# Performance work log

Hardware: AMD Instinct MI355X
Metric: run time of the kernel (lower is better)

Reference implementation:

```python
import jax, jax.numpy as jnp
import numpy as np

NUM_POINTS = 16384
OVERSAMPLE = 3
IMPORTANCE_RATIO = 0.75


def point_sample(feat, coords):
    """grid_sample(bilinear, align_corners=False, zero padding) at [0,1]^2 coords.
    feat: (N, C, H, W); coords: (N, P, 2) with coords[...,0]=x (width), [...,1]=y.
    Returns (N, C, P)."""
    N, C, H, W = feat.shape
    # grid_sample with g = 2c-1, align_corners=False -> pixel = c*size - 0.5
    x = coords[..., 0] * W - 0.5
    y = coords[..., 1] * H - 0.5
    x0 = jnp.floor(x)
    y0 = jnp.floor(y)
    x1 = x0 + 1.0
    y1 = y0 + 1.0
    wx1 = x - x0
    wx0 = 1.0 - wx1
    wy1 = y - y0
    wy0 = 1.0 - wy1
    featf = feat.reshape(N, C, H * W)

    def gather(yi, xi):
        valid = (xi >= 0) & (xi <= W - 1) & (yi >= 0) & (yi <= H - 1)
        xic = jnp.clip(xi, 0, W - 1).astype(jnp.int32)
        yic = jnp.clip(yi, 0, H - 1).astype(jnp.int32)
        idx = yic * W + xic  # (N, P)
        v = jnp.take_along_axis(featf, idx[:, None, :], axis=2)  # (N, C, P)
        return v * valid[:, None, :].astype(feat.dtype)

    out = (gather(y0, x0) * (wy0 * wx0)[:, None, :]
           + gather(y0, x1) * (wy0 * wx1)[:, None, :]
           + gather(y1, x0) * (wy1 * wx0)[:, None, :]
           + gather(y1, x1) * (wy1 * wx1)[:, None, :])
    return out


def calculate_uncertainty(logits):
    """logits: (N, C, P) -> (N, P) uncertainty = top2 - top1 (<= 0)."""
    if logits.shape[1] == 1:
        return -jnp.abs(logits)[:, 0, :]
    top2 = jax.lax.top_k(jnp.moveaxis(logits, 1, -1), 2)[0]  # (N, P, 2)
    return top2[..., 1] - top2[..., 0]


def sample_point_coords(coarse_logits):
    """get_uncertain_point_coords_with_randomness (torch.no_grad branch)."""
    N = coarse_logits.shape[0]
    num_sampled = NUM_POINTS * OVERSAMPLE
    num_imp = int(IMPORTANCE_RATIO * NUM_POINTS)
    num_rand = NUM_POINTS - num_imp
    k1, k2 = jax.random.split(jax.random.key(7))
    cand = jax.random.uniform(k1, (N, num_sampled, 2), dtype=jnp.float32)
    cand_logits = point_sample(coarse_logits, cand)  # (N, C, S)
    unc = calculate_uncertainty(cand_logits)  # (N, S)
    idx = jax.lax.top_k(unc, num_imp)[1]  # (N, num_imp)
    imp = jnp.take_along_axis(cand, idx[..., None], axis=1)  # (N, num_imp, 2)
    rand = jax.random.uniform(k2, (N, num_rand, 2), dtype=jnp.float32)
    return jnp.concatenate([imp, rand], axis=1)  # (N, P, 2)


def point_head(fine, coarse_pts, w0, b0, w1, b1, w2, b2, wp, bp):
    x = jnp.concatenate([fine, coarse_pts], axis=1)  # (N, nin+C, P)
    for w, b in ((w0, b0), (w1, b1), (w2, b2)):
        x = jax.nn.relu(jnp.einsum('oc,ncp->nop', w, x) + b[None, :, None])
        x = jnp.concatenate([x, coarse_pts], axis=1)  # coarse_pred_each_layer
    return jnp.einsum('oc,ncp->nop', wp, x) + bp[None, :, None]  # (N, C, P)


def setup_inputs() -> dict:
    key = jax.random.key(0)
    ks = jax.random.split(key, 8)
    N, C, Hc, Wc = 8, 19, 64, 64
    nin, Hf, Wf = 256, 128, 128
    fin = nin + C  # 275
    return {
        'coarse_sem_seg_logits': jax.random.normal(ks[0], (N, C, Hc, Wc), jnp.float32),
        'features': jax.random.normal(ks[1], (N, nin, Hf, Wf), jnp.float32),
        'w0': jax.random.normal(ks[2], (nin, fin), jnp.float32) * (2.0 / fin) ** 0.5,
        'b0': jnp.zeros((nin,), jnp.float32),
        'w1': jax.random.normal(ks[3], (nin, fin), jnp.float32) * (2.0 / fin) ** 0.5,
        'b1': jnp.zeros((nin,), jnp.float32),
        'w2': jax.random.normal(ks[4], (nin, fin), jnp.float32) * (2.0 / fin) ** 0.5,
        'b2': jnp.zeros((nin,), jnp.float32),
        'wp': jax.random.normal(ks[5], (C, fin), jnp.float32) * 0.001,
        'bp': jnp.zeros((C,), jnp.float32),
    }


def reference(coarse_sem_seg_logits, features, w0, b0, w1, b1, w2, b2, wp, bp):
    # training-mode forward of PointRendSemSegHead
    point_coords = jax.lax.stop_gradient(
        sample_point_coords(jax.lax.stop_gradient(coarse_sem_seg_logits)))
    coarse_pts = point_sample(coarse_sem_seg_logits, point_coords)  # (N, C, P)
    fine_pts = point_sample(features, point_coords)  # (N, nin, P)
    point_logits = point_head(fine_pts, coarse_pts, w0, b0, w1, b1, w2, b2, wp, bp)
    return coarse_sem_seg_logits, point_logits, point_coords
```

## Files before the change

kernel.cpp:

```cpp
#include <hip/hip_runtime.h>
#include <stdint.h>

#pragma clang fp contract(off)

#define NB    8
#define CCH   19
#define CSTR  20
#define FCH   256
#define FIN   275
#define KP    288
#define NPTS  16384
#define NSAMP 49152
#define NIMP  12288
#define NRAND 4096
#define SORT_M 65536
#define CHUNK  8192
#define TP    64
#define XROW  640
#define WBF_OFF (4u << 20)
#define CTR_OFF (4718592u)
#define FTR_OFF (8u << 20)
#define FTR_BYTES (134217728ull / 2)

typedef __attribute__((ext_vector_type(8))) short bf16x8;
typedef __attribute__((ext_vector_type(4))) float f32x4;

__host__ __device__ __forceinline__ uint32_t rotl32(uint32_t v, int r) {
  return (v << r) | (v >> (32 - r));
}

__host__ __device__ __forceinline__ void tf2x32(uint32_t k0, uint32_t k1,
                                                uint32_t x0, uint32_t x1,
                                                uint32_t* o0, uint32_t* o1) {
  const uint32_t ks2 = k0 ^ k1 ^ 0x1BD11BDAu;
  x0 += k0; x1 += k1;
#define TF_R(r) { x0 += x1; x1 = rotl32(x1, (r)); x1 ^= x0; }
  TF_R(13) TF_R(15) TF_R(26) TF_R(6)
  x0 += k1;  x1 += ks2 + 1u;
  TF_R(17) TF_R(29) TF_R(16) TF_R(24)
  x0 += ks2; x1 += k0 + 2u;
  TF_R(13) TF_R(15) TF_R(26) TF_R(6)
  x0 += k0;  x1 += k1 + 3u;
  TF_R(17) TF_R(29) TF_R(16) TF_R(24)
  x0 += k1;  x1 += ks2 + 4u;
  TF_R(13) TF_R(15) TF_R(26) TF_R(6)
  x0 += ks2; x1 += k0 + 5u;
#undef TF_R
  *o0 = x0; *o1 = x1;
}

__device__ __forceinline__ float u01_at(uint32_t k0, uint32_t k1, uint32_t i) {
  uint32_t o0, o1;
  tf2x32(k0, k1, 0u, i, &o0, &o1);
  const uint32_t b = o0 ^ o1;
  const float f = __uint_as_float((b >> 9) | 0x3f800000u) - 1.0f;
  return fmaxf(0.0f, f);
}

__device__ __forceinline__ unsigned short f2bf(float f) {
  const uint32_t u = __float_as_uint(f);
  return (unsigned short)((u + 0x7fffu + ((u >> 16) & 1u)) >> 16);
}

__device__ __forceinline__ float bf2f(unsigned short h) {
  return __uint_as_float((uint32_t)h << 16);
}

template <int SZ>
__device__ __forceinline__ void interp(float cx, float cy, int* off, float* wgt) {
  const float X = cx * (float)SZ - 0.5f, Y = cy * (float)SZ - 0.5f;
  const float x0f = floorf(X), y0f = floorf(Y);
  const float fx = X - x0f, fy = Y - y0f;
  const float wx0 = 1.0f - fx, wy0 = 1.0f - fy;
  const int x0 = (int)x0f, y0 = (int)y0f;
  const int x0c = min(max(x0, 0), SZ - 1), x1c = min(max(x0 + 1, 0), SZ - 1);
  const int y0c = min(max(y0, 0), SZ - 1), y1c = min(max(y0 + 1, 0), SZ - 1);
  const bool vx0 = (x0 >= 0) & (x0 <= SZ - 1), vx1 = (x0 >= -1) & (x0 <= SZ - 2);
  const bool vy0 = (y0 >= 0) & (y0 <= SZ - 1), vy1 = (y0 >= -1) & (y0 <= SZ - 2);
  off[0] = y0c * SZ + x0c; wgt[0] = (vy0 & vx0) ? wy0 * wx0 : 0.0f;
  off[1] = y0c * SZ + x1c; wgt[1] = (vy0 & vx1) ? wy0 * fx  : 0.0f;
  off[2] = y1c * SZ + x0c; wgt[2] = (vy1 & vx0) ? fy  * wx0 : 0.0f;
  off[3] = y1c * SZ + x1c; wgt[3] = (vy1 & vx1) ? fy  * fx  : 0.0f;
}

__global__ __launch_bounds__(256) void ctr_transpose(
    const float* __restrict__ coarse, float* __restrict__ ctr) {
  __shared__ float tile[CCH][257];
  const int b = blockIdx.x;
  const int nn = b >> 4, px0 = (b & 15) * 256;
  const int t = threadIdx.x;
  const float* src = coarse + (size_t)nn * (CCH * 4096) + px0;
#pragma unroll
  for (int c = 0; c < CCH; ++c) tile[c][t] = src[c * 4096 + t];
  __syncthreads();
  float v[CSTR];
#pragma unroll
  for (int c = 0; c < CCH; ++c) v[c] = tile[c][t];
  v[19] = 0.0f;
  float* dst = ctr + ((size_t)(nn << 12) + px0 + t) * CSTR;
#pragma unroll
  for (int k = 0; k < 5; ++k) {
    f32x4 x; x[0] = v[4*k]; x[1] = v[4*k+1]; x[2] = v[4*k+2]; x[3] = v[4*k+3];
    *(f32x4*)(dst + 4 * k) = x;
  }
}

__global__ __launch_bounds__(256) void fusedA(
    const float* __restrict__ feats, unsigned short* __restrict__ ftr,
    const float* __restrict__ ctr, unsigned long long* __restrict__ keys,
    const float* __restrict__ w0, const float* __restrict__ w1,
    const float* __restrict__ w2, const float* __restrict__ wpw,
    unsigned short* __restrict__ wbf, unsigned short* __restrict__ wpb,
    uint32_t k1a, uint32_t k1b, int use_tr) {
  __shared__ unsigned short tile[64][66];
  const int bid = blockIdx.x;
  const int t = threadIdx.x;

  if (bid < 8192) {
    if (!use_tr) return;
    const int nn = bid >> 10;
    const int ct = (bid >> 8) & 3;
    const int pt = bid & 255;
    const int c0 = ct * 64, p0 = pt * 64;
    const float* src = feats + ((size_t)nn << 22);
#pragma unroll 4
    for (int k = 0; k < 16; ++k) {
      const int c = 4 * k + (t >> 6);
      const int p = t & 63;
      tile[p][c] = f2bf(src[((size_t)(c0 + c) << 14) + p0 + p]);
    }
    __syncthreads();
    const int p = t >> 2, q = t & 3;
    const int cb = q * 16;
    uint32_t w[8];
#pragma unroll
    for (int m = 0; m < 8; ++m)
      w[m] = (uint32_t)tile[p][cb + 2 * m] | ((uint32_t)tile[p][cb + 2 * m + 1] << 16);
    unsigned short* dst = ftr + ((((size_t)nn << 14) + p0 + p) << 8) + c0 + cb;
    *(uint4*)(dst)     = make_uint4(w[0], w[1], w[2], w[3]);
    *(uint4*)(dst + 8) = make_uint4(w[4], w[5], w[6], w[7]);
  } else if (bid < 10240) {
    const int tid = (bid - 8192) * 256 + t;
    const int nn = tid >> 16, s = tid & (SORT_M - 1);
    if (s >= NSAMP) { keys[tid] = 0xFFFFFFFFFFFFFFFFull; return; }
    const uint32_t ci = (uint32_t)(((unsigned)nn * NSAMP + (unsigned)s) * 2);
    const float cx = u01_at(k1a, k1b, ci);
    const float cy = u01_at(k1a, k1b, ci + 1);
    const float X = cx * 64.0f - 0.5f, Y = cy * 64.0f - 0.5f;
    const float x0f = floorf(X), y0f = floorf(Y);
    const float fx = X - x0f, fy = Y - y0f;
    const float wx0 = 1.0f - fx, wy0 = 1.0f - fy;
    const int x0 = (int)x0f, y0 = (int)y0f;
    const int x0c = min(max(x0, 0), 63), x1c = min(max(x0 + 1, 0), 63);
    const int y0c = min(max(y0, 0), 63), y1c = min(max(y0 + 1, 0), 63);
    const bool vx0 = (x0 >= 0) & (x0 <= 63), vx1 = (x0 >= -1) & (x0 <= 62);
    const bool vy0 = (y0 >= 0) & (y0 <= 63), vy1 = (y0 >= -1) & (y0 <= 62);
    const float w00 = (vy0 & vx0) ? wy0 * wx0 : 0.0f;
    const float w01 = (vy0 & vx1) ? wy0 * fx  : 0.0f;
    const float w10 = (vy1 & vx0) ? fy  * wx0 : 0.0f;
    const float w11 = (vy1 & vx1) ? fy  * fx  : 0.0f;
    const float* rb = ctr + ((size_t)nn << 12) * CSTR;
    const float* r0 = rb + (size_t)(y0c * 64 + x0c) * CSTR;
    const float* r1 = rb + (size_t)(y0c * 64 + x1c) * CSTR;
    const float* r2 = rb + (size_t)(y1c * 64 + x0c) * CSTR;
    const float* r3 = rb + (size_t)(y1c * 64 + x1c) * CSTR;
    float m1 = -3.402823466e38f, m2 = -3.402823466e38f;
#pragma unroll
    for (int k = 0; k < 5; ++k) {
      const f32x4 x0v = *(const f32x4*)(r0 + 4 * k);
      const f32x4 x1v = *(const f32x4*)(r1 + 4 * k);
      const f32x4 x2v = *(const f32x4*)(r2 + 4 * k);
      const f32x4 x3v = *(const f32x4*)(r3 + 4 * k);
#pragma unroll
      for (int e = 0; e < 4; ++e) {
        const int c = 4 * k + e;
        if (c < CCH) {
          const float v = ((x0v[e] * w00 + x1v[e] * w01) + x2v[e] * w10) + x3v[e] * w11;
          if (v > m1) { m2 = m1; m1 = v; } else if (v > m2) { m2 = v; }
        }
      }
    }
    const float unc = m2 - m1;
    const uint32_t b = __float_as_uint(unc);
    const uint32_t asc = (b & 0x80000000u) ? ~b : (b | 0x80000000u);
    keys[tid] = ((unsigned long long)(~asc) << 32) | (uint32_t)s;
  } else {
    const int i = (bid - 10240) * 256 + t;
    if (i < 3 * 256 * KP) {
      const int L = i / (256 * KP);
      const int rem = i - L * (256 * KP);
      const int o = rem / KP, k = rem - o * KP;
      const float* W = (L == 0) ? w0 : (L == 1) ? w1 : w2;
      wbf[i] = (k < FIN) ? f2bf(W[o * FIN + k]) : (unsigned short)0;
    } else {
      const int j = i - 3 * 256 * KP;
      const int o = j / KP, k = j - o * KP;
      wpb[j] = (o < CCH && k < FIN) ? f2bf(wpw[o * FIN + k]) : (unsigned short)0;
    }
  }
}

__global__ __launch_bounds__(1024) void bitonic_local(unsigned long long* __restrict__ keys) {
  __shared__ unsigned long long s[CHUNK];
  const int cb = blockIdx.x;
  unsigned long long* a = keys + (size_t)cb * CHUNK;
  const unsigned gbase = (unsigned)(cb * CHUNK) & (SORT_M - 1);
  for (int i = threadIdx.x; i < CHUNK; i += 1024) s[i] = a[i];
  __syncthreads();
  for (int k = 2; k <= CHUNK; k <<= 1) {
    for (int j = k >> 1; j > 0; j >>= 1) {
      for (int pid = threadIdx.x; pid < CHUNK / 2; pid += 1024) {
        const int i = ((pid & ~(j - 1)) << 1) | (pid & (j - 1));
        const int l = i | j;
        const bool up = (((gbase + i) & k) == 0);
        const unsigned long long x = s[i], y = s[l];
        if ((x > y) == up) { s[i] = y; s[l] = x; }
      }
      __syncthreads();
    }
  }
  for (int i = threadIdx.x; i < CHUNK; i += 1024) a[i] = s[i];
}

__global__ __launch_bounds__(256) void bitonic_global(unsigned long long* __restrict__ keys,
                                                      int k, int j, int ppb_shift) {
  const int t = blockIdx.x * blockDim.x + threadIdx.x;
  const int b = t >> ppb_shift, pid = t & ((1 << ppb_shift) - 1);
  const int i = ((pid & ~(j - 1)) << 1) | (pid & (j - 1));
  const int l = i | j;
  const bool up = ((i & k) == 0);
  unsigned long long* a = keys + ((size_t)b << 16);
  const unsigned long long x = a[i], y = a[l];
  if ((x > y) == up) { a[i] = y; a[l] = x; }
}

__global__ __launch_bounds__(1024) void bitonic_finish(unsigned long long* __restrict__ keys,
                                                       int k) {
  __shared__ unsigned long long s[CHUNK];
  const int cb = blockIdx.x;
  unsigned long long* a = keys + (size_t)cb * CHUNK;
  const unsigned gi0 = (unsigned)(cb * CHUNK) & (SORT_M - 1);
  for (int i = threadIdx.x; i < CHUNK; i += 1024) s[i] = a[i];
  __syncthreads();
  const bool up = ((gi0 & k) == 0);
  for (int j = CHUNK >> 1; j > 0; j >>= 1) {
    for (int pid = threadIdx.x; pid < CHUNK / 2; pid += 1024) {
      const int i = ((pid & ~(j - 1)) << 1) | (pid & (j - 1));
      const int l = i | j;
      const unsigned long long x = s[i], y = s[l];
      if ((x > y) == up) { s[i] = y; s[l] = x; }
    }
    __syncthreads();
  }
  for (int i = threadIdx.x; i < CHUNK; i += 1024) a[i] = s[i];
}

__global__ __launch_bounds__(1024) void finlow_coords(
    const unsigned long long* __restrict__ keys, float* __restrict__ outc,
    uint32_t k1a, uint32_t k1b, uint32_t k2a, uint32_t k2b) {
  __shared__ unsigned long long s[CHUNK];
  const int nn = blockIdx.x >> 1, half = blockIdx.x & 1;
  const unsigned long long* a = keys + ((size_t)nn << 16) + half * CHUNK;
  for (int i = threadIdx.x; i < CHUNK; i += 1024) s[i] = a[i];
  __syncthreads();
  for (int j = CHUNK >> 1; j > 0; j >>= 1) {
    for (int pid = threadIdx.x; pid < CHUNK / 2; pid += 1024) {
      const int i = ((pid & ~(j - 1)) << 1) | (pid & (j - 1));
      const int l = i | j;
      const unsigned long long x = s[i], y = s[l];
      if (x > y) { s[i] = y; s[l] = x; }
    }
    __syncthreads();
  }
  const int pb = half * CHUNK;
  for (int q = threadIdx.x; q < CHUNK; q += 1024) {
    const int p = pb + q;
    float cx, cy;
    if (p < NIMP) {
      const unsigned idx = (unsigned)(s[q] & 0xFFFFFFFFu);
      const uint32_t ci = ((unsigned)nn * NSAMP + idx) * 2;
      cx = u01_at(k1a, k1b, ci);
      cy = u01_at(k1a, k1b, ci + 1);
    } else {
      const uint32_t ri = ((unsigned)nn * NRAND + (unsigned)(p - NIMP)) * 2;
      cx = u01_at(k2a, k2b, ri);
      cy = u01_at(k2a, k2b, ri + 1);
    }
    float* o = outc + (((size_t)nn << 14) + p) * 2;
    o[0] = cx; o[1] = cy;
  }
}

template <int USE_TR>
__global__ __launch_bounds__(512, 4) void fused_mfma(
    const float* __restrict__ coarse, const float* __restrict__ feats,
    const unsigned short* __restrict__ ftr, const float* __restrict__ ctr,
    const float* __restrict__ b0, const float* __restrict__ b1,
    const float* __restrict__ b2, const float* __restrict__ bp,
    const unsigned short* __restrict__ wbf, const unsigned short* __restrict__ wpb,
    const float* __restrict__ pc, float* __restrict__ outl) {
  __shared__ __align__(16) unsigned short xp[TP * (XROW / 2)];

  const int t = threadIdx.x;
  const int bid = ((int)blockIdx.x & 7) * 256 + ((int)blockIdx.x >> 3);
  const int nn = bid >> 8;
  const int pbase = (bid & 255) * TP;

  int offF[4]; float wgtF[4];
  int offC[4]; float wgtC[4];
  int offFc[4]; float wgtFc[4];
  {
    const float2 c = *(const float2*)(pc + ((size_t)nn * NPTS + pbase + (t >> 3)) * 2);
    interp<128>(c.x, c.y, offF, wgtF);
  }
  {
    const float2 c = *(const float2*)(pc + ((size_t)nn * NPTS + pbase + (t & 63)) * 2);
    interp<64>(c.x, c.y, offC, wgtC);
    if (!USE_TR) interp<128>(c.x, c.y, offFc, wgtFc);
  }

  if (USE_TR) {
    const int p = t >> 3, q = t & 7;
    const unsigned short* base = ftr + ((size_t)nn << 22) + q * 32;
    const unsigned short* n0 = base + ((size_t)offF[0] << 8);
    const unsigned short* n1 = base + ((size_t)offF[1] << 8);
    const unsigned short* n2 = base + ((size_t)offF[2] << 8);
    const unsigned short* n3 = base + ((size_t)offF[3] << 8);
    const float g0 = wgtF[0], g1 = wgtF[1], g2 = wgtF[2], g3 = wgtF[3];
    const unsigned swzp = (unsigned)(p & 7) << 4;
#pragma unroll
    for (int m = 0; m < 4; ++m) {
      const bf16x8 a = *(const bf16x8*)(n0 + m * 8);
      const bf16x8 bq = *(const bf16x8*)(n1 + m * 8);
      const bf16x8 c = *(const bf16x8*)(n2 + m * 8);
      const bf16x8 d = *(const bf16x8*)(n3 + m * 8);
      uint32_t u[4];
#pragma unroll
      for (int e = 0; e < 4; ++e) {
        float v0 = fmaf(bf2f((unsigned short)a[2 * e]), g0,
                   fmaf(bf2f((unsigned short)bq[2 * e]), g1,
                   fmaf(bf2f((unsigned short)c[2 * e]), g2,
                        bf2f((unsigned short)d[2 * e]) * g3)));
        float v1 = fmaf(bf2f((unsigned short)a[2 * e + 1]), g0,
                   fmaf(bf2f((unsigned short)bq[2 * e + 1]), g1,
                   fmaf(bf2f((unsigned short)c[2 * e + 1]), g2,
                        bf2f((unsigned short)d[2 * e + 1]) * g3)));
        u[e] = (uint32_t)f2bf(v0) | ((uint32_t)f2bf(v1) << 16);
      }
      *(uint4*)((char*)xp + p * XROW + (((unsigned)((q * 32 + m * 8) * 2)) ^ swzp)) =
          make_uint4(u[0], u[1], u[2], u[3]);
    }
    if (t < TP) {
      const int pp = t;
      const float* rb = ctr + ((size_t)nn << 12) * CSTR;
      const float* r0 = rb + (size_t)offC[0] * CSTR;
      const float* r1 = rb + (size_t)offC[1] * CSTR;
      const float* r2 = rb + (size_t)offC[2] * CSTR;
      const float* r3 = rb + (size_t)offC[3] * CSTR;
      const float h0 = wgtC[0], h1 = wgtC[1], h2 = wgtC[2], h3 = wgtC[3];
      unsigned short hs[32];
#pragma unroll
      for (int k = 0; k < 5; ++k) {
        const f32x4 x0v = *(const f32x4*)(r0 + 4 * k);
        const f32x4 x1v = *(const f32x4*)(r1 + 4 * k);
        const f32x4 x2v = *(const f32x4*)(r2 + 4 * k);
        const f32x4 x3v = *(const f32x4*)(r3 + 4 * k);
#pragma unroll
        for (int e = 0; e < 4; ++e) {
          const int c = 4 * k + e;
          if (c < CCH)
            hs[c] = f2bf(fmaf(x0v[e], h0, fmaf(x1v[e], h1,
                         fmaf(x2v[e], h2, x3v[e] * h3))));
        }
      }
#pragma unroll
      for (int c = CCH; c < 32; ++c) hs[c] = 0;
      const unsigned swzc = (unsigned)(pp & 7) << 4;
#pragma unroll
      for (int k = 0; k < 4; ++k) {
        uint4 u;
        u.x = (uint32_t)hs[8*k]   | ((uint32_t)hs[8*k+1] << 16);
        u.y = (uint32_t)hs[8*k+2] | ((uint32_t)hs[8*k+3] << 16);
        u.z = (uint32_t)hs[8*k+4] | ((uint32_t)hs[8*k+5] << 16);
        u.w = (uint32_t)hs[8*k+6] | ((uint32_t)hs[8*k+7] << 16);
        *(uint4*)((char*)xp + pp * XROW + (((unsigned)(512 + 16 * k)) ^ swzc)) = u;
      }
    }
  } else {
    for (int i = t; i < (KP / 2) * TP; i += 512) {
      const int p = i & (TP - 1);
      const int c0 = (i >> 6) * 2;
      float v0 = 0.0f, v1 = 0.0f;
      if (c0 < FCH) {
        const float* fb0 = feats + ((size_t)nn << 22) + ((size_t)c0 << 14);
        const float* fb1 = fb0 + 16384;
        v0 = ((fb0[offFc[0]] * wgtFc[0] + fb0[offFc[1]] * wgtFc[1])
             + fb0[offFc[2]] * wgtFc[2]) + fb0[offFc[3]] * wgtFc[3];
        v1 = ((fb1[offFc[0]] * wgtFc[0] + fb1[offFc[1]] * wgtFc[1])
             + fb1[offFc[2]] * wgtFc[2]) + fb1[offFc[3]] * wgtFc[3];
      } else if (c0 < FIN) {
        const float* cb0 = coarse + (size_t)nn * (CCH * 4096) + (size_t)(c0 - FCH) * 4096;
        v0 = ((cb0[offC[0]] * wgtC[0] + cb0[offC[1]] * wgtC[1])
             + cb0[offC[2]] * wgtC[2]) + cb0[offC[3]] * wgtC[3];
        if (c0 + 1 < FIN) {
          const float* cb1 = cb0 + 4096;
          v1 = ((cb1[offC[0]] * wgtC[0] + cb1[offC[1]] * wgtC[1])
               + cb1[offC[2]] * wgtC[2]) + cb1[offC[3]] * wgtC[3];
        }
      }
      const uint32_t u = (uint32_t)f2bf(v0) | ((uint32_t)f2bf(v1) << 16);
      *(uint32_t*)((char*)xp + p * XROW + (((unsigned)(c0 * 2)) ^ ((unsigned)(p & 7) << 4))) = u;
    }
  }

  const int lane = t & 63, wave = t >> 6;
  const int wm = wave & 3, wn = wave >> 2;
  const int l15 = lane & 15, g = lane >> 4;
  const unsigned swz = (unsigned)(l15 & 7) << 4;
  const char* xpB = (const char*)xp;

#pragma unroll
  for (int L = 0; L < 3; ++L) {
    __syncthreads();
    const float* Bv = (L == 0) ? b0 : (L == 1) ? b1 : b2;
    const unsigned short* wL = wbf + (size_t)L * (256 * KP);
    const unsigned short* wbase = wL + (size_t)(wm * 64 + l15) * KP + g * 8;

    f32x4 acc[4][2];
#pragma unroll
    for (int mt = 0; mt < 4; ++mt)
#pragma unroll
      for (int nt = 0; nt < 2; ++nt) acc[mt][nt] = (f32x4)(0.0f);

    bf16x8 a0 = *(const bf16x8*)(wbase + 0 * 16 * KP);
    bf16x8 a1 = *(const bf16x8*)(wbase + 1 * 16 * KP);
    bf16x8 a2 = *(const bf16x8*)(wbase + 2 * 16 * KP);
    bf16x8 a3 = *(const bf16x8*)(wbase + 3 * 16 * KP);
    for (int ks = 0; ks < 9; ++ks) {
      const bf16x8 c0v = a0, c1v = a1, c2v = a2, c3v = a3;
      if (ks < 8) {
        a0 = *(const bf16x8*)(wbase + 0 * 16 * KP + (ks + 1) * 32);
        a1 = *(const bf16x8*)(wbase + 1 * 16 * KP + (ks + 1) * 32);
        a2 = *(const bf16x8*)(wbase + 2 * 16 * KP + (ks + 1) * 32);
        a3 = *(const bf16x8*)(wbase + 3 * 16 * KP + (ks + 1) * 32);
      }
      const unsigned kb = (unsigned)(ks * 64 + g * 16) ^ swz;
      const bf16x8 q0 = *(const bf16x8*)(xpB + (wn * 32 + 0 + l15) * XROW + kb);
      const bf16x8 q1 = *(const bf16x8*)(xpB + (wn * 32 + 16 + l15) * XROW + kb);
      acc[0][0] = __builtin_amdgcn_mfma_f32_16x16x32_bf16(c0v, q0, acc[0][0], 0, 0, 0);
      acc[1][0] = __builtin_amdgcn_mfma_f32_16x16x32_bf16(c1v, q0, acc[1][0], 0, 0, 0);
      acc[2][0] = __builtin_amdgcn_mfma_f32_16x16x32_bf16(c2v, q0, acc[2][0], 0, 0, 0);
      acc[3][0] = __builtin_amdgcn_mfma_f32_16x16x32_bf16(c3v, q0, acc[3][0], 0, 0, 0);
      acc[0][1] = __builtin_amdgcn_mfma_f32_16x16x32_bf16(c0v, q1, acc[0][1], 0, 0, 0);
      acc[1][1] = __builtin_amdgcn_mfma_f32_16x16x32_bf16(c1v, q1, acc[1][1], 0, 0, 0);
      acc[2][1] = __builtin_amdgcn_mfma_f32_16x16x32_bf16(c2v, q1, acc[2][1], 0, 0, 0);
      acc[3][1] = __builtin_amdgcn_mfma_f32_16x16x32_bf16(c3v, q1, acc[3][1], 0, 0, 0);
    }
    __syncthreads();

#pragma unroll
    for (int mt = 0; mt < 4; ++mt) {
      const int ch0 = wm * 64 + mt * 16 + (g << 2);
      const float4 bv = *(const float4*)(Bv + ch0);
#pragma unroll
      for (int nt = 0; nt < 2; ++nt) {
        const int p = wn * 32 + nt * 16 + l15;
        const f32x4 v = acc[mt][nt];
        const unsigned short h0 = f2bf(fmaxf(v[0] + bv.x, 0.0f));
        const unsigned short h1 = f2bf(fmaxf(v[1] + bv.y, 0.0f));
        const unsigned short h2 = f2bf(fmaxf(v[2] + bv.z, 0.0f));
        const unsigned short h3 = f2bf(fmaxf(v[3] + bv.w, 0.0f));
        uint2 u;
        u.x = (uint32_t)h0 | ((uint32_t)h1 << 16);
        u.y = (uint32_t)h2 | ((uint32_t)h3 << 16);
        *(uint2*)((char*)xp + p * XROW + (((unsigned)(ch0 * 2)) ^ swz)) = u;
      }
    }
  }
  __syncthreads();

  const int hmt = wave >> 2, hnt = wave & 3;
  const unsigned short* hbase = wpb + (size_t)(hmt * 16 + l15) * KP + g * 8;
  f32x4 hacc = (f32x4)(0.0f);
  for (int ks = 0; ks < 9; ++ks) {
    const unsigned kb = (unsigned)(ks * 64 + g * 16) ^ swz;
    const bf16x8 ha = *(const bf16x8*)(hbase + ks * 32);
    const bf16x8 hb = *(const bf16x8*)(xpB + (hnt * 16 + l15) * XROW + kb);
    hacc = __builtin_amdgcn_mfma_f32_16x16x32_bf16(ha, hb, hacc, 0, 0, 0);
  }
  const int p = pbase + hnt * 16 + l15;
#pragma unroll
  for (int j = 0; j < 4; ++j) {
    const int ch = hmt * 16 + (g << 2) + j;
    if (ch < CCH)
      outl[((size_t)nn * CCH + ch) * NPTS + p] = hacc[j] + bp[ch];
  }
}

extern "C" void kernel_launch(void* const* d_in, const int* in_sizes, int n_in,
                              void* d_out, int out_size, void* d_ws, size_t ws_size,
                              hipStream_t stream) {
  const float* coarse = (const float*)d_in[0];
  const float* feats  = (const float*)d_in[1];
  const float* w0 = (const float*)d_in[2]; const float* b0 = (const float*)d_in[3];
  const float* w1 = (const float*)d_in[4]; const float* b1 = (const float*)d_in[5];
  const float* w2 = (const float*)d_in[6]; const float* b2 = (const float*)d_in[7];
  const float* wp = (const float*)d_in[8]; const float* bp = (const float*)d_in[9];

  float* out0 = (float*)d_out;
  float* outL = out0 + 622592;
  float* outC = outL + 2490368;

  unsigned long long* keys = (unsigned long long*)d_ws;
  unsigned short* wbf = (unsigned short*)((char*)d_ws + WBF_OFF);
  unsigned short* wpb = wbf + 3 * 256 * KP;
  float* ctr = (float*)((char*)d_ws + CTR_OFF);
  unsigned short* ftr = (unsigned short*)((char*)d_ws + FTR_OFF);
  const int use_tr = (ws_size >= (size_t)FTR_OFF + FTR_BYTES) ? 1 : 0;

  uint32_t k1a, k1b, k2a, k2b;
  tf2x32(0u, 7u, 0u, 0u, &k1a, &k1b);
  tf2x32(0u, 7u, 0u, 1u, &k2a, &k2b);

  hipMemcpyAsync(out0, coarse, 622592 * sizeof(float),
                 hipMemcpyDeviceToDevice, stream);

  ctr_transpose<<<128, 256, 0, stream>>>(coarse, ctr);

  fusedA<<<11140, 256, 0, stream>>>(feats, ftr, ctr, keys,
                                    w0, w1, w2, wp, wbf, wpb, k1a, k1b, use_tr);

  bitonic_local<<<64, 1024, 0, stream>>>(keys);
  bitonic_global<<<1024, 256, 0, stream>>>(keys, 16384, 8192, 15);
  bitonic_finish<<<64, 1024, 0, stream>>>(keys, 16384);
  bitonic_global<<<1024, 256, 0, stream>>>(keys, 32768, 16384, 15);
  bitonic_global<<<1024, 256, 0, stream>>>(keys, 32768, 8192, 15);
  bitonic_finish<<<64, 1024, 0, stream>>>(keys, 32768);
  bitonic_global<<<1024, 256, 0, stream>>>(keys, 65536, 32768, 15);
  bitonic_global<<<512, 256, 0, stream>>>(keys, 65536, 16384, 14);
  bitonic_global<<<256, 256, 0, stream>>>(keys, 65536, 8192, 13);
  finlow_coords<<<16, 1024, 0, stream>>>(keys, outC, k1a, k1b, k2a, k2b);

  if (use_tr)
    fused_mfma<1><<<2048, 512, 0, stream>>>(coarse, feats, ftr, ctr, b0, b1, b2,
                                            bp, wbf, wpb, outC, outL);
  else
    fused_mfma<0><<<2048, 512, 0, stream>>>(coarse, feats, ftr, ctr, b0, b1, b2,
                                            bp, wbf, wpb, outC, outL);
}
```

Baseline: 367.2 us.

## Spread feature transpose tiles across bitonic sort launches to fill idle CUs

The bf16 feature transpose (8192 tiles) is split into chunks and appended as extra blocks to each small sort kernel: uncertainty keys, local bitonic, global merges, finish and final coordinate extraction. Weight conversion is merged with the coarse transpose into a single prep kernel. The aim is to hide the bandwidth-bound transpose behind the latency-bound, low-occupancy sort stages. XROW also shrinks from 640 to 608, which reduces the LDS footprint of the MFMA kernel. The risk is that the extra blocks lengthen each sort stage on the critical path.

```diff
diff --git a/kernel.cpp b/kernel.cpp
--- a/kernel.cpp
+++ b/kernel.cpp
@@ -16,7 +16,7 @@
 #define SORT_M 65536
 #define CHUNK  8192
 #define TP    64
-#define XROW  640
+#define XROW  608
 #define WBF_OFF (4u << 20)
 #define CTR_OFF (4718592u)
 #define FTR_OFF (8u << 20)
@@ -83,64 +83,83 @@
   off[3] = y1c * SZ + x1c; wgt[3] = (vy1 & vx1) ? fy  * fx  : 0.0f;
 }
 
-__global__ __launch_bounds__(256) void ctr_transpose(
-    const float* __restrict__ coarse, float* __restrict__ ctr) {
-  __shared__ float tile[CCH][257];
-  const int b = blockIdx.x;
-  const int nn = b >> 4, px0 = (b & 15) * 256;
-  const int t = threadIdx.x;
-  const float* src = coarse + (size_t)nn * (CCH * 4096) + px0;
-#pragma unroll
-  for (int c = 0; c < CCH; ++c) tile[c][t] = src[c * 4096 + t];
-  __syncthreads();
-  float v[CSTR];
-#pragma unroll
-  for (int c = 0; c < CCH; ++c) v[c] = tile[c][t];
-  v[19] = 0.0f;
-  float* dst = ctr + ((size_t)(nn << 12) + px0 + t) * CSTR;
-#pragma unroll
-  for (int k = 0; k < 5; ++k) {
-    f32x4 x; x[0] = v[4*k]; x[1] = v[4*k+1]; x[2] = v[4*k+2]; x[3] = v[4*k+3];
-    *(f32x4*)(dst + 4 * k) = x;
-  }
-}
-
-__global__ __launch_bounds__(256) void fusedA(
-    const float* __restrict__ feats, unsigned short* __restrict__ ftr,
-    const float* __restrict__ ctr, unsigned long long* __restrict__ keys,
+__device__ __forceinline__ void ftr_tile_load(const float* __restrict__ feats,
+                                              int ti, int tt,
+                                              unsigned short (*tile)[66]) {
+  const int nn = ti >> 10, ct = (ti >> 8) & 3, pt = ti & 255;
+  const int c0 = ct * 64, p0 = pt * 64;
+  const float* src = feats + ((size_t)nn << 22);
+#pragma unroll 4
+  for (int k = 0; k < 16; ++k) {
+    const int c = 4 * k + (tt >> 6);
+    const int p = tt & 63;
+    tile[p][c] = f2bf(src[((size_t)(c0 + c) << 14) + p0 + p]);
+  }
+}
+
+__device__ __forceinline__ void ftr_tile_store(unsigned short* __restrict__ ftr,
+                                               int ti, int tt,
+                                               unsigned short (*tile)[66]) {
+  const int nn = ti >> 10, ct = (ti >> 8) & 3, pt = ti & 255;
+  const int c0 = ct * 64, p0 = pt * 64;
+  const int p = tt >> 2, q = tt & 3;
+  const int cb = q * 16;
+  uint32_t w[8];
+#pragma unroll
+  for (int m = 0; m < 8; ++m)
+    w[m] = (uint32_t)tile[p][cb + 2 * m] | ((uint32_t)tile[p][cb + 2 * m + 1] << 16);
+  unsigned short* dst = ftr + ((((size_t)nn << 14) + p0 + p) << 8) + c0 + cb;
+  *(uint4*)(dst)     = make_uint4(w[0], w[1], w[2], w[3]);
+  *(uint4*)(dst + 8) = make_uint4(w[4], w[5], w[6], w[7]);
+}
+
+__global__ __launch_bounds__(256) void prep(
+    const float* __restrict__ coarse, float* __restrict__ ctr,
     const float* __restrict__ w0, const float* __restrict__ w1,
     const float* __restrict__ w2, const float* __restrict__ wpw,
-    unsigned short* __restrict__ wbf, unsigned short* __restrict__ wpb,
-    uint32_t k1a, uint32_t k1b, int use_tr) {
+    unsigned short* __restrict__ wbf, unsigned short* __restrict__ wpb) {
+  __shared__ float tile[CCH][257];
+  const int b = blockIdx.x, t = threadIdx.x;
+  if (b < 128) {
+    const int nn = b >> 4, px0 = (b & 15) * 256;
+    const float* src = coarse + (size_t)nn * (CCH * 4096) + px0;
+#pragma unroll
+    for (int c = 0; c < CCH; ++c) tile[c][t] = src[c * 4096 + t];
+    __syncthreads();
+    float v[CSTR];
+#pragma unroll
+    for (int c = 0; c < CCH; ++c) v[c] = tile[c][t];
+    v[19] = 0.0f;
+    float* dst = ctr + ((size_t)(nn << 12) + px0 + t) * CSTR;
+#pragma unroll
+    for (int k = 0; k < 5; ++k) {
+      f32x4 x; x[0] = v[4*k]; x[1] = v[4*k+1]; x[2] = v[4*k+2]; x[3] = v[4*k+3];
+      *(f32x4*)(dst + 4 * k) = x;
+    }
+  } else {
+    const int i = (b - 128) * 256 + t;
+    if (i < 3 * 256 * KP) {
+      const int L = i / (256 * KP);
+      const int rem = i - L * (256 * KP);
+      const int o = rem / KP, k = rem - o * KP;
+      const float* W = (L == 0) ? w0 : (L == 1) ? w1 : w2;
+      wbf[i] = (k < FIN) ? f2bf(W[o * FIN + k]) : (unsigned short)0;
+    } else {
+      const int j = i - 3 * 256 * KP;
+      const int o = j / KP, k = j - o * KP;
+      wpb[j] = (o < CCH && k < FIN) ? f2bf(wpw[o * FIN + k]) : (unsigned short)0;
+    }
+  }
+}
+
+__global__ __launch_bounds__(256) void unc_tr(
+    const float* __restrict__ ctr, unsigned long long* __restrict__ keys,
+    const float* __restrict__ feats, unsigned short* __restrict__ ftr,
+    uint32_t k1a, uint32_t k1b, int tile0, int use_tr) {
   __shared__ unsigned short tile[64][66];
-  const int bid = blockIdx.x;
-  const int t = threadIdx.x;
-
-  if (bid < 8192) {
-    if (!use_tr) return;
-    const int nn = bid >> 10;
-    const int ct = (bid >> 8) & 3;
-    const int pt = bid & 255;
-    const int c0 = ct * 64, p0 = pt * 64;
-    const float* src = feats + ((size_t)nn << 22);
-#pragma unroll 4
-    for (int k = 0; k < 16; ++k) {
-      const int c = 4 * k + (t >> 6);
-      const int p = t & 63;
-      tile[p][c] = f2bf(src[((size_t)(c0 + c) << 14) + p0 + p]);
-    }
-    __syncthreads();
-    const int p = t >> 2, q = t & 3;
-    const int cb = q * 16;
-    uint32_t w[8];
-#pragma unroll
-    for (int m = 0; m < 8; ++m)
-      w[m] = (uint32_t)tile[p][cb + 2 * m] | ((uint32_t)tile[p][cb + 2 * m + 1] << 16);
-    unsigned short* dst = ftr + ((((size_t)nn << 14) + p0 + p) << 8) + c0 + cb;
-    *(uint4*)(dst)     = make_uint4(w[0], w[1], w[2], w[3]);
-    *(uint4*)(dst + 8) = make_uint4(w[4], w[5], w[6], w[7]);
-  } else if (bid < 10240) {
-    const int tid = (bid - 8192) * 256 + t;
+  const int bid = blockIdx.x, t = threadIdx.x;
+  if (bid < 2048) {
+    const int tid = bid * 256 + t;
     const int nn = tid >> 16, s = tid & (SORT_M - 1);
     if (s >= NSAMP) { keys[tid] = 0xFFFFFFFFFFFFFFFFull; return; }
     const uint32_t ci = (uint32_t)(((unsigned)nn * NSAMP + (unsigned)s) * 2);
@@ -185,109 +204,155 @@
     const uint32_t asc = (b & 0x80000000u) ? ~b : (b | 0x80000000u);
     keys[tid] = ((unsigned long long)(~asc) << 32) | (uint32_t)s;
   } else {
-    const int i = (bid - 10240) * 256 + t;
-    if (i < 3 * 256 * KP) {
-      const int L = i / (256 * KP);
-      const int rem = i - L * (256 * KP);
-      const int o = rem / KP, k = rem - o * KP;
-      const float* W = (L == 0) ? w0 : (L == 1) ? w1 : w2;
-      wbf[i] = (k < FIN) ? f2bf(W[o * FIN + k]) : (unsigned short)0;
-    } else {
-      const int j = i - 3 * 256 * KP;
-      const int o = j / KP, k = j - o * KP;
-      wpb[j] = (o < CCH && k < FIN) ? f2bf(wpw[o * FIN + k]) : (unsigned short)0;
-    }
-  }
-}
-
-__global__ __launch_bounds__(1024) void bitonic_local(unsigned long long* __restrict__ keys) {
+    if (!use_tr) return;
+    const int ti = tile0 + (bid - 2048);
+    ftr_tile_load(feats, ti, t, tile);
+    __syncthreads();
+    ftr_tile_store(ftr, ti, t, tile);
+  }
+}
+
+__global__ __launch_bounds__(1024) void bitonic_local_tr(
+    unsigned long long* __restrict__ keys,
+    const float* __restrict__ feats, unsigned short* __restrict__ ftr,
+    int tile0, int use_tr) {
   __shared__ unsigned long long s[CHUNK];
-  const int cb = blockIdx.x;
-  unsigned long long* a = keys + (size_t)cb * CHUNK;
-  const unsigned gbase = (unsigned)(cb * CHUNK) & (SORT_M - 1);
-  for (int i = threadIdx.x; i < CHUNK; i += 1024) s[i] = a[i];
-  __syncthreads();
-  for (int k = 2; k <= CHUNK; k <<= 1) {
-    for (int j = k >> 1; j > 0; j >>= 1) {
-      for (int pid = threadIdx.x; pid < CHUNK / 2; pid += 1024) {
+  const int b = blockIdx.x, t = threadIdx.x;
+  if (b < 64) {
+    unsigned long long* a = keys + (size_t)b * CHUNK;
+    const unsigned gbase = (unsigned)(b * CHUNK) & (SORT_M - 1);
+    for (int i = t; i < CHUNK; i += 1024) s[i] = a[i];
+    __syncthreads();
+    for (int k = 2; k <= CHUNK; k <<= 1) {
+      for (int j = k >> 1; j > 0; j >>= 1) {
+        for (int pid = t; pid < CHUNK / 2; pid += 1024) {
+          const int i = ((pid & ~(j - 1)) << 1) | (pid & (j - 1));
+          const int l = i | j;
+          const bool up = (((gbase + i) & k) == 0);
+          const unsigned long long x = s[i], y = s[l];
+          if ((x > y) == up) { s[i] = y; s[l] = x; }
+        }
+        __syncthreads();
+      }
+    }
+    for (int i = t; i < CHUNK; i += 1024) a[i] = s[i];
+  } else {
+    if (!use_tr) return;
+    unsigned short (*tp)[66] =
+        (unsigned short (*)[66])((char*)s + (size_t)(t >> 8) * (64 * 66 * 2));
+    const int ti = tile0 + (b - 64) * 4 + (t >> 8);
+    const int tt = t & 255;
+    ftr_tile_load(feats, ti, tt, tp);
+    __syncthreads();
+    ftr_tile_store(ftr, ti, tt, tp);
+  }
+}
+
+__global__ __launch_bounds__(256) void bitonic_global_tr(
+    unsigned long long* __restrict__ keys, int k, int j, int ppb_shift, int nsort,
+    const float* __restrict__ feats, unsigned short* __restrict__ ftr,
+    int tile0, int use_tr) {
+  __shared__ unsigned short tile[64][66];
+  const int bb = blockIdx.x, tt = threadIdx.x;
+  if (bb < nsort) {
+    const int t = bb * 256 + tt;
+    const int b = t >> ppb_shift, pid = t & ((1 << ppb_shift) - 1);
+    const int i = ((pid & ~(j - 1)) << 1) | (pid & (j - 1));
+    const int l = i | j;
+    const bool up = ((i & k) == 0);
+    unsigned long long* a = keys + ((size_t)b << 16);
+    const unsigned long long x = a[i], y = a[l];
+    if ((x > y) == up) { a[i] = y; a[l] = x; }
+  } else {
+    if (!use_tr) return;
+    const int ti = tile0 + (bb - nsort);
+    ftr_tile_load(feats, ti, tt, tile);
+    __syncthreads();
+    ftr_tile_store(ftr, ti, tt, tile);
+  }
+}
+
+__global__ __launch_bounds__(1024) void bitonic_finish_tr(
+    unsigned long long* __restrict__ keys, int k,
+    const float* __restrict__ feats, unsigned short* __restrict__ ftr,
+    int tile0, int use_tr) {
+  __shared__ unsigned long long s[CHUNK];
+  const int b = blockIdx.x, t = threadIdx.x;
+  if (b < 64) {
+    unsigned long long* a = keys + (size_t)b * CHUNK;
+    const unsigned gi0 = (unsigned)(b * CHUNK) & (SORT_M - 1);
+    for (int i = t; i < CHUNK; i += 1024) s[i] = a[i];
+    __syncthreads();
+    const bool up = ((gi0 & k) == 0);
+    for (int j = CHUNK >> 1; j > 0; j >>= 1) {
+      for (int pid = t; pid < CHUNK / 2; pid += 1024) {
         const int i = ((pid & ~(j - 1)) << 1) | (pid & (j - 1));
         const int l = i | j;
-        const bool up = (((gbase + i) & k) == 0);
         const unsigned long long x = s[i], y = s[l];
         if ((x > y) == up) { s[i] = y; s[l] = x; }
       }
       __syncthreads();
     }
-  }
-  for (int i = threadIdx.x; i < CHUNK; i += 1024) a[i] = s[i];
-}
-
-__global__ __launch_bounds__(256) void bitonic_global(unsigned long long* __restrict__ keys,
-                                                      int k, int j, int ppb_shift) {
-  const int t = blockIdx.x * blockDim.x + threadIdx.x;
-  const int b = t >> ppb_shift, pid = t & ((1 << ppb_shift) - 1);
-  const int i = ((pid & ~(j - 1)) << 1) | (pid & (j - 1));
-  const int l = i | j;
-  const bool up = ((i & k) == 0);
-  unsigned long long* a = keys + ((size_t)b << 16);
-  const unsigned long long x = a[i], y = a[l];
-  if ((x > y) == up) { a[i] = y; a[l] = x; }
-}
-
-__global__ __launch_bounds__(1024) void bitonic_finish(unsigned long long* __restrict__ keys,
-                                                       int k) {
+    for (int i = t; i < CHUNK; i += 1024) a[i] = s[i];
+  } else {
+    if (!use_tr) return;
+    unsigned short (*tp)[66] =
+        (unsigned short (*)[66])((char*)s + (size_t)(t >> 8) * (64 * 66 * 2));
+    const int ti = tile0 + (b - 64) * 4 + (t >> 8);
+    const int tt = t & 255;
+    ftr_tile_load(feats, ti, tt, tp);
+    __syncthreads();
+    ftr_tile_store(ftr, ti, tt, tp);
+  }
+}
+
+__global__ __launch_bounds__(1024) void finlow_tr(
+    const unsigned long long* __restrict__ keys, float* __restrict__ outc,
+    uint32_t k1a, uint32_t k1b, uint32_t k2a, uint32_t k2b,
+    const float* __restrict__ feats, unsigned short* __restrict__ ftr,
+    int tile0, int use_tr) {
   __shared__ unsigned long long s[CHUNK];
-  const int cb = blockIdx.x;
-  unsigned long long* a = keys + (size_t)cb * CHUNK;
-  const unsigned gi0 = (unsigned)(cb * CHUNK) & (SORT_M - 1);
-  for (int i = threadIdx.x; i < CHUNK; i += 1024) s[i] = a[i];
-  __syncthreads();
-  const bool up = ((gi0 & k) == 0);
-  for (int j = CHUNK >> 1; j > 0; j >>= 1) {
-    for (int pid = threadIdx.x; pid < CHUNK / 2; pid += 1024) {
-      const int i = ((pid & ~(j - 1)) << 1) | (pid & (j - 1));
-      const int l = i | j;
-      const unsigned long long x = s[i], y = s[l];
-      if ((x > y) == up) { s[i] = y; s[l] = x; }
-    }
-    __syncthreads();
-  }
-  for (int i = threadIdx.x; i < CHUNK; i += 1024) a[i] = s[i];
-}
-
-__global__ __launch_bounds__(1024) void finlow_coords(
-    const unsigned long long* __restrict__ keys, float* __restrict__ outc,
-    uint32_t k1a, uint32_t k1b, uint32_t k2a, uint32_t k2b) {
-  __shared__ unsigned long long s[CHUNK];
-  const int nn = blockIdx.x >> 1, half = blockIdx.x & 1;
-  const unsigned long long* a = keys + ((size_t)nn << 16) + half * CHUNK;
-  for (int i = threadIdx.x; i < CHUNK; i += 1024) s[i] = a[i];
-  __syncthreads();
-  for (int j = CHUNK >> 1; j > 0; j >>= 1) {
-    for (int pid = threadIdx.x; pid < CHUNK / 2; pid += 1024) {
-      const int i = ((pid & ~(j - 1)) << 1) | (pid & (j - 1));
-      const int l = i | j;
-      const unsigned long long x = s[i], y = s[l];
-      if (x > y) { s[i] = y; s[l] = x; }
-    }
-    __syncthreads();
-  }
-  const int pb = half * CHUNK;
-  for (int q = threadIdx.x; q < CHUNK; q += 1024) {
-    const int p = pb + q;
-    float cx, cy;
-    if (p < NIMP) {
-      const unsigned idx = (unsigned)(s[q] & 0xFFFFFFFFu);
-      const uint32_t ci = ((unsigned)nn * NSAMP + idx) * 2;
-      cx = u01_at(k1a, k1b, ci);
-      cy = u01_at(k1a, k1b, ci + 1);
-    } else {
-      const uint32_t ri = ((unsigned)nn * NRAND + (unsigned)(p - NIMP)) * 2;
-      cx = u01_at(k2a, k2b, ri);
-      cy = u01_at(k2a, k2b, ri + 1);
-    }
-    float* o = outc + (((size_t)nn << 14) + p) * 2;
-    o[0] = cx; o[1] = cy;
+  const int b = blockIdx.x, t = threadIdx.x;
+  if (b < 16) {
+    const int nn = b >> 1, half = b & 1;
+    const unsigned long long* a = keys + ((size_t)nn << 16) + half * CHUNK;
+    for (int i = t; i < CHUNK; i += 1024) s[i] = a[i];
+    __syncthreads();
+    for (int j = CHUNK >> 1; j > 0; j >>= 1) {
+      for (int pid = t; pid < CHUNK / 2; pid += 1024) {
+        const int i = ((pid & ~(j - 1)) << 1) | (pid & (j - 1));
+        const int l = i | j;
+        const unsigned long long x = s[i], y = s[l];
+        if (x > y) { s[i] = y; s[l] = x; }
+      }
+      __syncthreads();
+    }
+    const int pb = half * CHUNK;
+    for (int q = t; q < CHUNK; q += 1024) {
+      const int p = pb + q;
+      float cx, cy;
+      if (p < NIMP) {
+        const unsigned idx = (unsigned)(s[q] & 0xFFFFFFFFu);
+        const uint32_t ci = ((unsigned)nn * NSAMP + idx) * 2;
+        cx = u01_at(k1a, k1b, ci);
+        cy = u01_at(k1a, k1b, ci + 1);
+      } else {
+        const uint32_t ri = ((unsigned)nn * NRAND + (unsigned)(p - NIMP)) * 2;
+        cx = u01_at(k2a, k2b, ri);
+        cy = u01_at(k2a, k2b, ri + 1);
+      }
+      float* o = outc + (((size_t)nn << 14) + p) * 2;
+      o[0] = cx; o[1] = cy;
+    }
+  } else {
+    if (!use_tr) return;
+    unsigned short (*tp)[66] =
+        (unsigned short (*)[66])((char*)s + (size_t)(t >> 8) * (64 * 66 * 2));
+    const int ti = tile0 + (b - 16) * 4 + (t >> 8);
+    const int tt = t & 255;
+    ftr_tile_load(feats, ti, tt, tp);
+    __syncthreads();
+    ftr_tile_store(ftr, ti, tt, tp);
   }
 }
 
@@ -525,21 +590,30 @@
   hipMemcpyAsync(out0, coarse, 622592 * sizeof(float),
                  hipMemcpyDeviceToDevice, stream);
 
-  ctr_transpose<<<128, 256, 0, stream>>>(coarse, ctr);
-
-  fusedA<<<11140, 256, 0, stream>>>(feats, ftr, ctr, keys,
-                                    w0, w1, w2, wp, wbf, wpb, k1a, k1b, use_tr);
-
-  bitonic_local<<<64, 1024, 0, stream>>>(keys);
-  bitonic_global<<<1024, 256, 0, stream>>>(keys, 16384, 8192, 15);
-  bitonic_finish<<<64, 1024, 0, stream>>>(keys, 16384);
-  bitonic_global<<<1024, 256, 0, stream>>>(keys, 32768, 16384, 15);
-  bitonic_global<<<1024, 256, 0, stream>>>(keys, 32768, 8192, 15);
-  bitonic_finish<<<64, 1024, 0, stream>>>(keys, 32768);
-  bitonic_global<<<1024, 256, 0, stream>>>(keys, 65536, 32768, 15);
-  bitonic_global<<<512, 256, 0, stream>>>(keys, 65536, 16384, 14);
-  bitonic_global<<<256, 256, 0, stream>>>(keys, 65536, 8192, 13);
-  finlow_coords<<<16, 1024, 0, stream>>>(keys, outC, k1a, k1b, k2a, k2b);
+  prep<<<1028, 256, 0, stream>>>(coarse, ctr, w0, w1, w2, wp, wbf, wpb);
+
+  const int NT = use_tr ? 1 : 0;
+  unc_tr<<<2048 + NT * 1024, 256, 0, stream>>>(ctr, keys, feats, ftr,
+                                               k1a, k1b, 0, use_tr);
+  bitonic_local_tr<<<64 + NT * 192, 1024, 0, stream>>>(keys, feats, ftr, 1024, use_tr);
+  bitonic_global_tr<<<1024 + NT * 896, 256, 0, stream>>>(keys, 16384, 8192, 15, 1024,
+                                                         feats, ftr, 1792, use_tr);
+  bitonic_finish_tr<<<64 + NT * 112, 1024, 0, stream>>>(keys, 16384, feats, ftr,
+                                                        2688, use_tr);
+  bitonic_global_tr<<<1024 + NT * 896, 256, 0, stream>>>(keys, 32768, 16384, 15, 1024,
+                                                         feats, ftr, 3136, use_tr);
+  bitonic_global_tr<<<1024 + NT * 896, 256, 0, stream>>>(keys, 32768, 8192, 15, 1024,
+                                                         feats, ftr, 4032, use_tr);
+  bitonic_finish_tr<<<64 + NT * 112, 1024, 0, stream>>>(keys, 32768, feats, ftr,
+                                                        4928, use_tr);
+  bitonic_global_tr<<<1024 + NT * 896, 256, 0, stream>>>(keys, 65536, 32768, 15, 1024,
+                                                         feats, ftr, 5376, use_tr);
+  bitonic_global_tr<<<512 + NT * 896, 256, 0, stream>>>(keys, 65536, 16384, 14, 512,
+                                                        feats, ftr, 6272, use_tr);
+  bitonic_global_tr<<<256 + NT * 896, 256, 0, stream>>>(keys, 65536, 8192, 13, 256,
+                                                        feats, ftr, 7168, use_tr);
+  finlow_tr<<<16 + NT * 32, 1024, 0, stream>>>(keys, outC, k1a, k1b, k2a, k2b,
+                                               feats, ftr, 8064, use_tr);
 
   if (use_tr)
     fused_mfma<1><<<2048, 512, 0, stream>>>(coarse, feats, ftr, ctr, b0, b1, b2,
```

Result: no change. 361.2 us (-1.6%).
